# Kernel tuning notes

Hardware: AMD Instinct MI355X
Metric: run time of the kernel (lower is better)

## Reference

```python
import jax, jax.numpy as jnp
import numpy as np

B, T, D, H, O = 256, 512, 256, 1024, 128


def setup_inputs() -> dict:
    key = jax.random.key(0)
    ks = jax.random.split(key, 16)
    s_x = 1.0 / np.sqrt(D)
    s_h = 1.0 / np.sqrt(H)
    def lin(k, shape, s):
        return jax.random.uniform(k, shape, jnp.float32, -s, s)
    return {
        "x": jax.random.normal(ks[0], (B, T, D), jnp.float32),
        "Wgx": lin(ks[1], (H, D), s_x), "bgx": lin(ks[2], (H,), s_x),
        "Wgh": lin(ks[3], (H, H), s_h),
        "Wix": lin(ks[4], (H, D), s_x), "bix": lin(ks[5], (H,), s_x),
        "Wih": lin(ks[6], (H, H), s_h),
        "Wfx": lin(ks[7], (H, D), s_x), "bfx": lin(ks[8], (H,), s_x),
        "Wfh": lin(ks[9], (H, H), s_h),
        "Wox": lin(ks[10], (H, D), s_x), "box": lin(ks[11], (H,), s_x),
        "Woh": lin(ks[12], (H, H), s_h),
        "Why": lin(ks[13], (O, H), s_h), "bhy": lin(ks[14], (O,), s_h),
    }


def _lstm_forward(x, Wgx, bgx, Wgh, Wix, bix, Wih, Wfx, bfx, Wfh, Wox, box, Woh, Why, bhy):
    # Precompute all input-side projections in one big GEMM: [B,T,4H]
    Wx = jnp.concatenate([Wgx, Wix, Wfx, Wox], axis=0)          # [4H, D]
    bx = jnp.concatenate([bgx, bix, bfx, box], axis=0)          # [4H]
    Wh = jnp.concatenate([Wgh, Wih, Wfh, Woh], axis=0)          # [4H, H]
    xz = jnp.einsum('btd,kd->tbk', x, Wx) + bx                  # [T,B,4H]

    Hd = Wgh.shape[0]

    def step(carry, xz_t):
        h, c = carry
        z = xz_t + h @ Wh.T                                     # [B,4H]
        g = jnp.tanh(z[:, :Hd])
        i = jax.nn.sigmoid(z[:, Hd:2 * Hd])
        f = jax.nn.sigmoid(z[:, 2 * Hd:3 * Hd])
        o = jax.nn.sigmoid(z[:, 3 * Hd:])
        c = g * i + c * f
        h = jnp.tanh(c) * o
        return (h, c), None

    h0 = jnp.zeros((x.shape[0], Hd), x.dtype)
    c0 = jnp.zeros((x.shape[0], Hd), x.dtype)
    (h, _), _ = jax.lax.scan(step, (h0, c0), xz)
    p = h @ Why.T + bhy
    return jax.nn.softmax(p, axis=-1)


def reference(x, Wgx, bgx, Wgh, Wix, bix, Wih, Wfx, bfx, Wfh, Wox, box, Woh, Why, bhy):
    return _lstm_forward(x, Wgx, bgx, Wgh, Wix, bix, Wih, Wfx, bfx, Wfh, Wox, box, Woh, Why, bhy)
```

## Files before the change

### kernel.cpp

```cpp
#include <hip/hip_runtime.h>
#include <math.h>

#define B_  256
#define T_  512
#define D_  256
#define H_  1024
#define O_  128
#define N4H 4096

typedef __attribute__((ext_vector_type(8))) short bf16x8;
typedef __attribute__((ext_vector_type(4))) float f32x4;

__device__ __forceinline__ unsigned short f2bf(float x) {
    union { float f; unsigned u; } v; v.f = x;
    unsigned r = v.u + 0x7fffu + ((v.u >> 16) & 1u);
    return (unsigned short)(r >> 16);
}
__device__ __forceinline__ float bf2f(unsigned short b) {
    union { float f; unsigned u; } v; v.u = ((unsigned)b) << 16;
    return v.f;
}
__device__ __forceinline__ void splitf(float w, short& hi, short& lo) {
    union { float f; unsigned u; } v; v.f = w;
    union { float f; unsigned u; } hf; hf.u = v.u & 0xffff0000u;
    hi = (short)(unsigned short)(v.u >> 16);
    lo = (short)f2bf(w - hf.f);
}

__global__ __launch_bounds__(256) void pack_weights(
    const float* __restrict__ Wgx, const float* __restrict__ bgx, const float* __restrict__ Wgh,
    const float* __restrict__ Wix, const float* __restrict__ bix, const float* __restrict__ Wih,
    const float* __restrict__ Wfx, const float* __restrict__ bfx, const float* __restrict__ Wfh,
    const float* __restrict__ Wox, const float* __restrict__ box, const float* __restrict__ Woh,
    unsigned short* __restrict__ Whhi, unsigned short* __restrict__ Whlo,
    unsigned short* __restrict__ WXhi, unsigned short* __restrict__ WXlo,
    float* __restrict__ biasP)
{
    int idx = blockIdx.x * 256 + threadIdx.x;
    const int K = H_ + D_;
    const int total = N4H * K;
    if (idx < total) {
        int np = idx / K;
        int k  = idx - np * K;
        int j = np >> 2, g = np & 3;
        const float* Wh = (g == 0) ? Wgh : (g == 1) ? Wih : (g == 2) ? Wfh : Woh;
        const float* Wx = (g == 0) ? Wgx : (g == 1) ? Wix : (g == 2) ? Wfx : Wox;
        float w = (k < H_) ? Wh[j * H_ + k] : Wx[j * D_ + (k - H_)];
        unsigned short hi = f2bf(w);
        unsigned short lo = f2bf(w - bf2f(hi));
        if (k < H_) { Whhi[np * H_ + k] = hi; Whlo[np * H_ + k] = lo; }
        else        { WXhi[np * D_ + (k - H_)] = hi; WXlo[np * D_ + (k - H_)] = lo; }
    }
    if (idx < N4H) {
        int j = idx >> 2, g = idx & 3;
        const float* bx = (g == 0) ? bgx : (g == 1) ? bix : (g == 2) ? bfx : box;
        biasP[idx] = bx[j];
    }
}

__global__ __launch_bounds__(256, 2) void xz_gemm(
    const float* __restrict__ x,
    const unsigned short* __restrict__ WXhi, const unsigned short* __restrict__ WXlo,
    const float* __restrict__ biasP,
    float* __restrict__ xz, int t0)
{
    const int tid  = threadIdx.x;
    const int wave = tid >> 6;
    const int lane = tid & 63;
    const int lrow = lane & 15;
    const int quad = lane >> 4;
    const int wr = wave >> 1, wc = wave & 1;

    const int cg    = blockIdx.x;
    const int t_rel = blockIdx.y >> 1;
    const int bhalf = blockIdx.y & 1;
    const int t     = t0 + t_rel;

    const int b0 = bhalf * 128 + wr * 64;
    const int n0 = cg * 128 + wc * 64;

    f32x4 acc[4][4];
    #pragma unroll
    for (int rs = 0; rs < 4; ++rs)
        #pragma unroll
        for (int cs = 0; cs < 4; ++cs)
            acc[rs][cs] = (f32x4){0.f, 0.f, 0.f, 0.f};

    #pragma unroll 1
    for (int kc = 0; kc < D_; kc += 32) {
        bf16x8 Ahi[4], Alo[4], Bh[4], Bl[4];
        #pragma unroll
        for (int rs = 0; rs < 4; ++rs) {
            int b = b0 + rs * 16 + lrow;
            const float* p = x + (size_t)b * (T_ * D_) + (size_t)t * D_ + kc + quad * 8;
            float4 v0 = *(const float4*)p;
            float4 v1 = *(const float4*)(p + 4);
            float vv[8] = {v0.x, v0.y, v0.z, v0.w, v1.x, v1.y, v1.z, v1.w};
            #pragma unroll
            for (int j = 0; j < 8; ++j) {
                short hi, lo; splitf(vv[j], hi, lo);
                Ahi[rs][j] = hi; Alo[rs][j] = lo;
            }
        }
        #pragma unroll
        for (int cs = 0; cs < 4; ++cs) {
            int rw = n0 + cs * 16 + lrow;
            int off = rw * D_ + kc + quad * 8;
            Bh[cs] = *(const bf16x8*)(WXhi + off);
            Bl[cs] = *(const bf16x8*)(WXlo + off);
        }
        #pragma unroll
        for (int rs = 0; rs < 4; ++rs)
            #pragma unroll
            for (int cs = 0; cs < 4; ++cs) {
                acc[rs][cs] = __builtin_amdgcn_mfma_f32_16x16x32_bf16(Ahi[rs], Bh[cs], acc[rs][cs], 0, 0, 0);
                acc[rs][cs] = __builtin_amdgcn_mfma_f32_16x16x32_bf16(Ahi[rs], Bl[cs], acc[rs][cs], 0, 0, 0);
                acc[rs][cs] = __builtin_amdgcn_mfma_f32_16x16x32_bf16(Alo[rs], Bh[cs], acc[rs][cs], 0, 0, 0);
            }
    }

    #pragma unroll
    for (int cs = 0; cs < 4; ++cs) {
        int col = n0 + cs * 16 + lrow;
        float bv = biasP[col];
        #pragma unroll
        for (int rs = 0; rs < 4; ++rs) {
            int row0 = b0 + rs * 16 + quad * 4;
            #pragma unroll
            for (int r = 0; r < 4; ++r)
                xz[(size_t)(t_rel * B_ + row0 + r) * N4H + col] = acc[rs][cs][r] + bv;
        }
    }
}

__global__ __launch_bounds__(512, 2) void lstm_step(
    const unsigned short* __restrict__ Whhi, const unsigned short* __restrict__ Whlo,
    const unsigned short* __restrict__ hin_hi, const unsigned short* __restrict__ hin_lo,
    unsigned short* __restrict__ hout_hi, unsigned short* __restrict__ hout_lo,
    float* __restrict__ cst, const float* __restrict__ xz, int t_rel)
{
    __shared__ __align__(16) float zbuf[8][64][68];

    const int tid  = threadIdx.x;
    const int wave = tid >> 6;
    const int lane = tid & 63;
    const int lrow = lane & 15;
    const int quad = lane >> 4;

    const int fid = blockIdx.x;
    const int xcd = fid & 7;
    const int s   = fid >> 3;
    const int cg  = xcd * 8 + (s & 7);
    const int rg  = s >> 3;
    const int rbase = rg * 64;
    const int cbase = cg * 64;

    f32x4 acc[4][4];
    #pragma unroll
    for (int rs = 0; rs < 4; ++rs)
        #pragma unroll
        for (int cs = 0; cs < 4; ++cs)
            acc[rs][cs] = (f32x4){0.f, 0.f, 0.f, 0.f};

    const int kb = wave * 128;
    #pragma unroll 2
    for (int kc = 0; kc < 128; kc += 32) {
        const int k = kb + kc + quad * 8;
        bf16x8 Ahi[4], Alo[4], Bh[4], Bl[4];
        #pragma unroll
        for (int rs = 0; rs < 4; ++rs) {
            int off = (rbase + rs * 16 + lrow) * H_ + k;
            Ahi[rs] = *(const bf16x8*)(hin_hi + off);
            Alo[rs] = *(const bf16x8*)(hin_lo + off);
        }
        #pragma unroll
        for (int cs = 0; cs < 4; ++cs) {
            int off = (cbase + cs * 16 + lrow) * H_ + k;
            Bh[cs] = *(const bf16x8*)(Whhi + off);
            Bl[cs] = *(const bf16x8*)(Whlo + off);
        }
        #pragma unroll
        for (int rs = 0; rs < 4; ++rs)
            #pragma unroll
            for (int cs = 0; cs < 4; ++cs) {
                acc[rs][cs] = __builtin_amdgcn_mfma_f32_16x16x32_bf16(Ahi[rs], Bh[cs], acc[rs][cs], 0, 0, 0);
                acc[rs][cs] = __builtin_amdgcn_mfma_f32_16x16x32_bf16(Ahi[rs], Bl[cs], acc[rs][cs], 0, 0, 0);
                acc[rs][cs] = __builtin_amdgcn_mfma_f32_16x16x32_bf16(Alo[rs], Bh[cs], acc[rs][cs], 0, 0, 0);
            }
    }

    #pragma unroll
    for (int rs = 0; rs < 4; ++rs)
        #pragma unroll
        for (int cs = 0; cs < 4; ++cs)
            #pragma unroll
            for (int r = 0; r < 4; ++r)
                zbuf[wave][rs * 16 + quad * 4 + r][cs * 16 + lrow] = acc[rs][cs][r];
    __syncthreads();

    const int b_loc = tid >> 3;
    const int oc    = (tid & 7) * 8;

    float zz[8];
    #pragma unroll
    for (int i = 0; i < 8; i += 4) {
        float s0 = 0.f, s1 = 0.f, s2 = 0.f, s3 = 0.f;
        #pragma unroll
        for (int w = 0; w < 8; ++w) {
            float4 v = *(const float4*)&zbuf[w][b_loc][oc + i];
            s0 += v.x; s1 += v.y; s2 += v.z; s3 += v.w;
        }
        zz[i] = s0; zz[i + 1] = s1; zz[i + 2] = s2; zz[i + 3] = s3;
    }

    const int b = rbase + b_loc;
    const size_t xzoff = ((size_t)t_rel * B_ + b) * N4H + cbase + oc;
    float4 xa = *(const float4*)(xz + xzoff);
    float4 xb = *(const float4*)(xz + xzoff + 4);
    zz[0] += xa.x; zz[1] += xa.y; zz[2] += xa.z; zz[3] += xa.w;
    zz[4] += xb.x; zz[5] += xb.y; zz[6] += xb.z; zz[7] += xb.w;

    const int j0 = cg * 16 + (tid & 7) * 2;
    float2 cold = *(const float2*)&cst[b * H_ + j0];
    float coldv[2] = {cold.x, cold.y};

    float cnew[2];
    unsigned short hh[2], hl[2];
    #pragma unroll
    for (int j = 0; j < 2; ++j) {
        float zg = zz[4 * j + 0];
        float zi = zz[4 * j + 1];
        float zf = zz[4 * j + 2];
        float zo = zz[4 * j + 3];
        float g  = tanhf(zg);
        float ig = 1.f / (1.f + expf(-zi));
        float fg = 1.f / (1.f + expf(-zf));
        float og = 1.f / (1.f + expf(-zo));
        float cn = g * ig + coldv[j] * fg;
        float hn = tanhf(cn) * og;
        cnew[j] = cn;
        unsigned short h16 = f2bf(hn);
        hh[j] = h16;
        hl[j] = f2bf(hn - bf2f(h16));
    }
    *(float2*)&cst[b * H_ + j0] = make_float2(cnew[0], cnew[1]);
    *(ushort2*)&hout_hi[b * H_ + j0] = make_ushort2(hh[0], hh[1]);
    *(ushort2*)&hout_lo[b * H_ + j0] = make_ushort2(hl[0], hl[1]);
}

__global__ __launch_bounds__(128) void final_proj(
    const unsigned short* __restrict__ hhi, const unsigned short* __restrict__ hlo,
    const float* __restrict__ Why, const float* __restrict__ bhy,
    float* __restrict__ out)
{
    __shared__ float hsh[H_];
    __shared__ float red[O_];
    const int b = blockIdx.x, tid = threadIdx.x;

    for (int k = tid; k < H_; k += O_)
        hsh[k] = bf2f(hhi[(size_t)b * H_ + k]) + bf2f(hlo[(size_t)b * H_ + k]);
    __syncthreads();

    float s = bhy[tid];
    const float* w = Why + (size_t)tid * H_;
    #pragma unroll 4
    for (int k = 0; k < H_; k += 4) {
        float4 wv = *(const float4*)(w + k);
        s += hsh[k] * wv.x + hsh[k + 1] * wv.y + hsh[k + 2] * wv.z + hsh[k + 3] * wv.w;
    }

    red[tid] = s; __syncthreads();
    for (int off = 64; off > 0; off >>= 1) {
        if (tid < off) red[tid] = fmaxf(red[tid], red[tid + off]);
        __syncthreads();
    }
    float mx = red[0]; __syncthreads();
    float e = expf(s - mx);
    red[tid] = e; __syncthreads();
    for (int off = 64; off > 0; off >>= 1) {
        if (tid < off) red[tid] += red[tid + off];
        __syncthreads();
    }
    out[(size_t)b * O_ + tid] = e / red[0];
}

extern "C" void kernel_launch(void* const* d_in, const int* in_sizes, int n_in,
                              void* d_out, int out_size, void* d_ws, size_t ws_size,
                              hipStream_t stream)
{
    const float* x   = (const float*)d_in[0];
    const float* Wgx = (const float*)d_in[1];
    const float* bgx = (const float*)d_in[2];
    const float* Wgh = (const float*)d_in[3];
    const float* Wix = (const float*)d_in[4];
    const float* bix = (const float*)d_in[5];
    const float* Wih = (const float*)d_in[6];
    const float* Wfx = (const float*)d_in[7];
    const float* bfx = (const float*)d_in[8];
    const float* Wfh = (const float*)d_in[9];
    const float* Wox = (const float*)d_in[10];
    const float* box = (const float*)d_in[11];
    const float* Woh = (const float*)d_in[12];
    const float* Why = (const float*)d_in[13];
    const float* bhy = (const float*)d_in[14];

    unsigned short* Whhi = (unsigned short*)d_ws;
    unsigned short* Whlo = Whhi + (size_t)N4H * H_;
    unsigned short* WXhi = Whlo + (size_t)N4H * H_;
    unsigned short* WXlo = WXhi + (size_t)N4H * D_;
    float*          bP   = (float*)(WXlo + (size_t)N4H * D_);
    unsigned short* hA_hi = (unsigned short*)(bP + N4H);
    unsigned short* hA_lo = hA_hi + (size_t)B_ * H_;
    float*          cst   = (float*)(hA_lo + (size_t)B_ * H_);
    unsigned short* hB_hi = (unsigned short*)(cst + (size_t)B_ * H_);
    unsigned short* hB_lo = hB_hi + (size_t)B_ * H_;
    float*          xz    = (float*)(hB_lo + (size_t)B_ * H_);

    const size_t fixed_bytes = (size_t)((char*)xz - (char*)d_ws);
    const size_t per_t = (size_t)B_ * N4H * sizeof(float);
    int Tc = 1;
    if (ws_size > fixed_bytes) {
        size_t fit = (ws_size - fixed_bytes) / per_t;
        Tc = (fit > 64) ? 64 : (fit < 1 ? 1 : (int)fit);
    }

    hipMemsetAsync(hA_hi, 0, (size_t)B_ * H_ * 8, stream);

    const int totalW = N4H * (H_ + D_);
    pack_weights<<<(totalW + 255) / 256, 256, 0, stream>>>(
        Wgx, bgx, Wgh, Wix, bix, Wih, Wfx, bfx, Wfh, Wox, box, Woh,
        Whhi, Whlo, WXhi, WXlo, bP);

    for (int t0 = 0; t0 < T_; t0 += Tc) {
        const int tc = (T_ - t0 < Tc) ? (T_ - t0) : Tc;
        xz_gemm<<<dim3(32, 2 * tc), 256, 0, stream>>>(x, WXhi, WXlo, bP, xz, t0);
        for (int t = t0; t < t0 + tc; ++t) {
            const unsigned short* ih = (t & 1) ? hB_hi : hA_hi;
            const unsigned short* il = (t & 1) ? hB_lo : hA_lo;
            unsigned short* oh = (t & 1) ? hA_hi : hB_hi;
            unsigned short* ol = (t & 1) ? hA_lo : hB_lo;
            lstm_step<<<256, 512, 0, stream>>>(
                Whhi, Whlo, ih, il, oh, ol, cst, xz, t - t0);
        }
    }

    final_proj<<<B_, 128, 0, stream>>>(hA_hi, hA_lo, Why, bhy, (float*)d_out);
}
```

Baseline: 11.96 ms.

## Fuse LSTM timesteps and input GEMM into persistent cooperative kernel

Replaces the per-chunk input-projection launches and the per-timestep step launches with one cooperative persistent kernel. Each block first computes the input projections for its own batch-row and gate-column tile, then loops over timesteps. Steps are separated by a global-memory atomic barrier that only spans the 64 blocks sharing a batch-row group, since the recurrence never mixes batch rows. The cell state now stays in registers instead of round-tripping through global memory. The aim is to remove kernel launch and inter-kernel drain overhead. In exchange it adds spin-wait barrier latency, and it relies on all 256 blocks being co-resident.

```diff
diff --git a/kernel.cpp b/kernel.cpp
--- a/kernel.cpp
+++ b/kernel.cpp
@@ -58,194 +58,205 @@
     }
 }
 
-__global__ __launch_bounds__(256, 2) void xz_gemm(
+__global__ __launch_bounds__(512, 2) void lstm_persistent(
     const float* __restrict__ x,
+    const unsigned short* __restrict__ Whhi, const unsigned short* __restrict__ Whlo,
     const unsigned short* __restrict__ WXhi, const unsigned short* __restrict__ WXlo,
     const float* __restrict__ biasP,
-    float* __restrict__ xz, int t0)
+    unsigned short* __restrict__ h0hi, unsigned short* __restrict__ h0lo,
+    unsigned short* __restrict__ h1hi, unsigned short* __restrict__ h1lo,
+    float* __restrict__ xz,
+    unsigned int* __restrict__ bar,
+    int Tc)
 {
+    __shared__ __align__(16) float zbuf[8][64][68];
+
     const int tid  = threadIdx.x;
     const int wave = tid >> 6;
     const int lane = tid & 63;
     const int lrow = lane & 15;
     const int quad = lane >> 4;
-    const int wr = wave >> 1, wc = wave & 1;
-
-    const int cg    = blockIdx.x;
-    const int t_rel = blockIdx.y >> 1;
-    const int bhalf = blockIdx.y & 1;
-    const int t     = t0 + t_rel;
-
-    const int b0 = bhalf * 128 + wr * 64;
-    const int n0 = cg * 128 + wc * 64;
-
-    f32x4 acc[4][4];
-    #pragma unroll
-    for (int rs = 0; rs < 4; ++rs)
-        #pragma unroll
-        for (int cs = 0; cs < 4; ++cs)
-            acc[rs][cs] = (f32x4){0.f, 0.f, 0.f, 0.f};
-
-    #pragma unroll 1
-    for (int kc = 0; kc < D_; kc += 32) {
-        bf16x8 Ahi[4], Alo[4], Bh[4], Bl[4];
-        #pragma unroll
-        for (int rs = 0; rs < 4; ++rs) {
-            int b = b0 + rs * 16 + lrow;
-            const float* p = x + (size_t)b * (T_ * D_) + (size_t)t * D_ + kc + quad * 8;
-            float4 v0 = *(const float4*)p;
-            float4 v1 = *(const float4*)(p + 4);
-            float vv[8] = {v0.x, v0.y, v0.z, v0.w, v1.x, v1.y, v1.z, v1.w};
-            #pragma unroll
-            for (int j = 0; j < 8; ++j) {
-                short hi, lo; splitf(vv[j], hi, lo);
-                Ahi[rs][j] = hi; Alo[rs][j] = lo;
-            }
-        }
-        #pragma unroll
-        for (int cs = 0; cs < 4; ++cs) {
-            int rw = n0 + cs * 16 + lrow;
-            int off = rw * D_ + kc + quad * 8;
-            Bh[cs] = *(const bf16x8*)(WXhi + off);
-            Bl[cs] = *(const bf16x8*)(WXlo + off);
-        }
-        #pragma unroll
-        for (int rs = 0; rs < 4; ++rs)
-            #pragma unroll
-            for (int cs = 0; cs < 4; ++cs) {
-                acc[rs][cs] = __builtin_amdgcn_mfma_f32_16x16x32_bf16(Ahi[rs], Bh[cs], acc[rs][cs], 0, 0, 0);
-                acc[rs][cs] = __builtin_amdgcn_mfma_f32_16x16x32_bf16(Ahi[rs], Bl[cs], acc[rs][cs], 0, 0, 0);
-                acc[rs][cs] = __builtin_amdgcn_mfma_f32_16x16x32_bf16(Alo[rs], Bh[cs], acc[rs][cs], 0, 0, 0);
-            }
-    }
-
-    #pragma unroll
-    for (int cs = 0; cs < 4; ++cs) {
-        int col = n0 + cs * 16 + lrow;
-        float bv = biasP[col];
-        #pragma unroll
-        for (int rs = 0; rs < 4; ++rs) {
-            int row0 = b0 + rs * 16 + quad * 4;
-            #pragma unroll
-            for (int r = 0; r < 4; ++r)
-                xz[(size_t)(t_rel * B_ + row0 + r) * N4H + col] = acc[rs][cs][r] + bv;
-        }
-    }
-}
-
-__global__ __launch_bounds__(512, 2) void lstm_step(
-    const unsigned short* __restrict__ Whhi, const unsigned short* __restrict__ Whlo,
-    const unsigned short* __restrict__ hin_hi, const unsigned short* __restrict__ hin_lo,
-    unsigned short* __restrict__ hout_hi, unsigned short* __restrict__ hout_lo,
-    float* __restrict__ cst, const float* __restrict__ xz, int t_rel)
-{
-    __shared__ __align__(16) float zbuf[8][64][68];
-
-    const int tid  = threadIdx.x;
-    const int wave = tid >> 6;
-    const int lane = tid & 63;
-    const int lrow = lane & 15;
-    const int quad = lane >> 4;
 
     const int fid = blockIdx.x;
     const int xcd = fid & 7;
     const int s   = fid >> 3;
-    const int cg  = xcd * 8 + (s & 7);
+    const int cgi = xcd * 8 + (s & 7);
     const int rg  = s >> 3;
     const int rbase = rg * 64;
-    const int cbase = cg * 64;
-
-    f32x4 acc[4][4];
-    #pragma unroll
-    for (int rs = 0; rs < 4; ++rs)
-        #pragma unroll
-        for (int cs = 0; cs < 4; ++cs)
-            acc[rs][cs] = (f32x4){0.f, 0.f, 0.f, 0.f};
-
-    const int kb = wave * 128;
-    #pragma unroll 2
-    for (int kc = 0; kc < 128; kc += 32) {
-        const int k = kb + kc + quad * 8;
-        bf16x8 Ahi[4], Alo[4], Bh[4], Bl[4];
-        #pragma unroll
-        for (int rs = 0; rs < 4; ++rs) {
-            int off = (rbase + rs * 16 + lrow) * H_ + k;
-            Ahi[rs] = *(const bf16x8*)(hin_hi + off);
-            Alo[rs] = *(const bf16x8*)(hin_lo + off);
-        }
-        #pragma unroll
-        for (int cs = 0; cs < 4; ++cs) {
-            int off = (cbase + cs * 16 + lrow) * H_ + k;
-            Bh[cs] = *(const bf16x8*)(Whhi + off);
-            Bl[cs] = *(const bf16x8*)(Whlo + off);
-        }
-        #pragma unroll
-        for (int rs = 0; rs < 4; ++rs)
-            #pragma unroll
-            for (int cs = 0; cs < 4; ++cs) {
-                acc[rs][cs] = __builtin_amdgcn_mfma_f32_16x16x32_bf16(Ahi[rs], Bh[cs], acc[rs][cs], 0, 0, 0);
-                acc[rs][cs] = __builtin_amdgcn_mfma_f32_16x16x32_bf16(Ahi[rs], Bl[cs], acc[rs][cs], 0, 0, 0);
-                acc[rs][cs] = __builtin_amdgcn_mfma_f32_16x16x32_bf16(Alo[rs], Bh[cs], acc[rs][cs], 0, 0, 0);
-            }
-    }
-
-    #pragma unroll
-    for (int rs = 0; rs < 4; ++rs)
-        #pragma unroll
-        for (int cs = 0; cs < 4; ++cs)
-            #pragma unroll
-            for (int r = 0; r < 4; ++r)
-                zbuf[wave][rs * 16 + quad * 4 + r][cs * 16 + lrow] = acc[rs][cs][r];
-    __syncthreads();
+    const int cbase = cgi * 64;
 
     const int b_loc = tid >> 3;
     const int oc    = (tid & 7) * 8;
-
-    float zz[8];
-    #pragma unroll
-    for (int i = 0; i < 8; i += 4) {
-        float s0 = 0.f, s1 = 0.f, s2 = 0.f, s3 = 0.f;
-        #pragma unroll
-        for (int w = 0; w < 8; ++w) {
-            float4 v = *(const float4*)&zbuf[w][b_loc][oc + i];
-            s0 += v.x; s1 += v.y; s2 += v.z; s3 += v.w;
+    const int bown  = rbase + b_loc;
+    const int j0    = cgi * 16 + (tid & 7) * 2;
+    float c0 = 0.f, c1 = 0.f;
+
+    unsigned int* const mybar = bar + rg * 32;
+    unsigned int barTarget = 0;
+
+    for (int t0 = 0; t0 < T_; t0 += Tc) {
+        const int tc = (T_ - t0 < Tc) ? (T_ - t0) : Tc;
+
+        for (int t_rel = wave; t_rel < tc; t_rel += 8) {
+            const int t = t0 + t_rel;
+            f32x4 acc[4][4];
+            #pragma unroll
+            for (int rs = 0; rs < 4; ++rs)
+                #pragma unroll
+                for (int cs = 0; cs < 4; ++cs)
+                    acc[rs][cs] = (f32x4){0.f, 0.f, 0.f, 0.f};
+
+            #pragma unroll 1
+            for (int kc = 0; kc < D_; kc += 32) {
+                bf16x8 Ahi[4], Alo[4], Bh[4], Bl[4];
+                #pragma unroll
+                for (int rs = 0; rs < 4; ++rs) {
+                    int b = rbase + rs * 16 + lrow;
+                    const float* p = x + (size_t)b * (T_ * D_) + (size_t)t * D_ + kc + quad * 8;
+                    float4 v0 = *(const float4*)p;
+                    float4 v1 = *(const float4*)(p + 4);
+                    float vv[8] = {v0.x, v0.y, v0.z, v0.w, v1.x, v1.y, v1.z, v1.w};
+                    #pragma unroll
+                    for (int j = 0; j < 8; ++j) {
+                        short hi, lo; splitf(vv[j], hi, lo);
+                        Ahi[rs][j] = hi; Alo[rs][j] = lo;
+                    }
+                }
+                #pragma unroll
+                for (int cs = 0; cs < 4; ++cs) {
+                    int off = (cbase + cs * 16 + lrow) * D_ + kc + quad * 8;
+                    Bh[cs] = *(const bf16x8*)(WXhi + off);
+                    Bl[cs] = *(const bf16x8*)(WXlo + off);
+                }
+                #pragma unroll
+                for (int rs = 0; rs < 4; ++rs)
+                    #pragma unroll
+                    for (int cs = 0; cs < 4; ++cs) {
+                        acc[rs][cs] = __builtin_amdgcn_mfma_f32_16x16x32_bf16(Ahi[rs], Bh[cs], acc[rs][cs], 0, 0, 0);
+                        acc[rs][cs] = __builtin_amdgcn_mfma_f32_16x16x32_bf16(Ahi[rs], Bl[cs], acc[rs][cs], 0, 0, 0);
+                        acc[rs][cs] = __builtin_amdgcn_mfma_f32_16x16x32_bf16(Alo[rs], Bh[cs], acc[rs][cs], 0, 0, 0);
+                    }
+            }
+            #pragma unroll
+            for (int cs = 0; cs < 4; ++cs) {
+                int col = cbase + cs * 16 + lrow;
+                float bv = biasP[col];
+                #pragma unroll
+                for (int rs = 0; rs < 4; ++rs) {
+                    int row0 = rbase + rs * 16 + quad * 4;
+                    #pragma unroll
+                    for (int r = 0; r < 4; ++r)
+                        xz[(size_t)(t_rel * B_ + row0 + r) * N4H + col] = acc[rs][cs][r] + bv;
+                }
+            }
         }
-        zz[i] = s0; zz[i + 1] = s1; zz[i + 2] = s2; zz[i + 3] = s3;
-    }
-
-    const int b = rbase + b_loc;
-    const size_t xzoff = ((size_t)t_rel * B_ + b) * N4H + cbase + oc;
-    float4 xa = *(const float4*)(xz + xzoff);
-    float4 xb = *(const float4*)(xz + xzoff + 4);
-    zz[0] += xa.x; zz[1] += xa.y; zz[2] += xa.z; zz[3] += xa.w;
-    zz[4] += xb.x; zz[5] += xb.y; zz[6] += xb.z; zz[7] += xb.w;
-
-    const int j0 = cg * 16 + (tid & 7) * 2;
-    float2 cold = *(const float2*)&cst[b * H_ + j0];
-    float coldv[2] = {cold.x, cold.y};
-
-    float cnew[2];
-    unsigned short hh[2], hl[2];
-    #pragma unroll
-    for (int j = 0; j < 2; ++j) {
-        float zg = zz[4 * j + 0];
-        float zi = zz[4 * j + 1];
-        float zf = zz[4 * j + 2];
-        float zo = zz[4 * j + 3];
-        float g  = tanhf(zg);
-        float ig = 1.f / (1.f + expf(-zi));
-        float fg = 1.f / (1.f + expf(-zf));
-        float og = 1.f / (1.f + expf(-zo));
-        float cn = g * ig + coldv[j] * fg;
-        float hn = tanhf(cn) * og;
-        cnew[j] = cn;
-        unsigned short h16 = f2bf(hn);
-        hh[j] = h16;
-        hl[j] = f2bf(hn - bf2f(h16));
-    }
-    *(float2*)&cst[b * H_ + j0] = make_float2(cnew[0], cnew[1]);
-    *(ushort2*)&hout_hi[b * H_ + j0] = make_ushort2(hh[0], hh[1]);
-    *(ushort2*)&hout_lo[b * H_ + j0] = make_ushort2(hl[0], hl[1]);
+
+        for (int t_rel = 0; t_rel < tc; ++t_rel) {
+            const int t = t0 + t_rel;
+            const unsigned short* ih = (t & 1) ? h1hi : h0hi;
+            const unsigned short* il = (t & 1) ? h1lo : h0lo;
+            unsigned short* oh = (t & 1) ? h0hi : h1hi;
+            unsigned short* ol = (t & 1) ? h0lo : h1lo;
+
+            f32x4 acc[4][4];
+            #pragma unroll
+            for (int rs = 0; rs < 4; ++rs)
+                #pragma unroll
+                for (int cs = 0; cs < 4; ++cs)
+                    acc[rs][cs] = (f32x4){0.f, 0.f, 0.f, 0.f};
+
+            const int kb = wave * 128;
+            #pragma unroll 2
+            for (int kc = 0; kc < 128; kc += 32) {
+                const int k = kb + kc + quad * 8;
+                bf16x8 Ahi[4], Alo[4], Bh[4], Bl[4];
+                #pragma unroll
+                for (int rs = 0; rs < 4; ++rs) {
+                    int off = (rbase + rs * 16 + lrow) * H_ + k;
+                    Ahi[rs] = *(const bf16x8*)(ih + off);
+                    Alo[rs] = *(const bf16x8*)(il + off);
+                }
+                #pragma unroll
+                for (int cs = 0; cs < 4; ++cs) {
+                    int off = (cbase + cs * 16 + lrow) * H_ + k;
+                    Bh[cs] = *(const bf16x8*)(Whhi + off);
+                    Bl[cs] = *(const bf16x8*)(Whlo + off);
+                }
+                #pragma unroll
+                for (int rs = 0; rs < 4; ++rs)
+                    #pragma unroll
+                    for (int cs = 0; cs < 4; ++cs) {
+                        acc[rs][cs] = __builtin_amdgcn_mfma_f32_16x16x32_bf16(Ahi[rs], Bh[cs], acc[rs][cs], 0, 0, 0);
+                        acc[rs][cs] = __builtin_amdgcn_mfma_f32_16x16x32_bf16(Ahi[rs], Bl[cs], acc[rs][cs], 0, 0, 0);
+                        acc[rs][cs] = __builtin_amdgcn_mfma_f32_16x16x32_bf16(Alo[rs], Bh[cs], acc[rs][cs], 0, 0, 0);
+                    }
+            }
+
+            #pragma unroll
+            for (int rs = 0; rs < 4; ++rs)
+                #pragma unroll
+                for (int cs = 0; cs < 4; ++cs)
+                    #pragma unroll
+                    for (int r = 0; r < 4; ++r)
+                        zbuf[wave][rs * 16 + quad * 4 + r][cs * 16 + lrow] = acc[rs][cs][r];
+            __syncthreads();
+
+            float zz[8];
+            #pragma unroll
+            for (int i = 0; i < 8; i += 4) {
+                float s0 = 0.f, s1 = 0.f, s2 = 0.f, s3 = 0.f;
+                #pragma unroll
+                for (int w = 0; w < 8; ++w) {
+                    float4 v = *(const float4*)&zbuf[w][b_loc][oc + i];
+                    s0 += v.x; s1 += v.y; s2 += v.z; s3 += v.w;
+                }
+                zz[i] = s0; zz[i + 1] = s1; zz[i + 2] = s2; zz[i + 3] = s3;
+            }
+
+            const size_t xzoff = ((size_t)t_rel * B_ + bown) * N4H + cbase + oc;
+            float4 xa = *(const float4*)(xz + xzoff);
+            float4 xb = *(const float4*)(xz + xzoff + 4);
+            zz[0] += xa.x; zz[1] += xa.y; zz[2] += xa.z; zz[3] += xa.w;
+            zz[4] += xb.x; zz[5] += xb.y; zz[6] += xb.z; zz[7] += xb.w;
+
+            float cold[2] = {c0, c1};
+            unsigned short hh[2], hl[2];
+            float cnew[2];
+            #pragma unroll
+            for (int j = 0; j < 2; ++j) {
+                float zg = zz[4 * j + 0];
+                float zi = zz[4 * j + 1];
+                float zf = zz[4 * j + 2];
+                float zo = zz[4 * j + 3];
+                float g  = tanhf(zg);
+                float ig = 1.f / (1.f + expf(-zi));
+                float fg = 1.f / (1.f + expf(-zf));
+                float og = 1.f / (1.f + expf(-zo));
+                float cn = g * ig + cold[j] * fg;
+                float hn = tanhf(cn) * og;
+                cnew[j] = cn;
+                unsigned short h16 = f2bf(hn);
+                hh[j] = h16;
+                hl[j] = f2bf(hn - bf2f(h16));
+            }
+            c0 = cnew[0]; c1 = cnew[1];
+            *(ushort2*)&oh[bown * H_ + j0] = make_ushort2(hh[0], hh[1]);
+            *(ushort2*)&ol[bown * H_ + j0] = make_ushort2(hl[0], hl[1]);
+
+            if (t != T_ - 1) {
+                barTarget += 64;
+                if (tid == 0) {
+                    __threadfence();
+                    atomicAdd(mybar, 1u);
+                    while (__hip_atomic_load(mybar, __ATOMIC_RELAXED,
+                                             __HIP_MEMORY_SCOPE_AGENT) < barTarget)
+                        __builtin_amdgcn_s_sleep(1);
+                    __threadfence();
+                }
+            }
+            __syncthreads();
+        }
+    }
 }
 
 __global__ __launch_bounds__(128) void final_proj(
@@ -309,10 +320,10 @@
     unsigned short* WXhi = Whlo + (size_t)N4H * H_;
     unsigned short* WXlo = WXhi + (size_t)N4H * D_;
     float*          bP   = (float*)(WXlo + (size_t)N4H * D_);
-    unsigned short* hA_hi = (unsigned short*)(bP + N4H);
+    unsigned int*   bars = (unsigned int*)(bP + N4H);
+    unsigned short* hA_hi = (unsigned short*)(bars + 128);
     unsigned short* hA_lo = hA_hi + (size_t)B_ * H_;
-    float*          cst   = (float*)(hA_lo + (size_t)B_ * H_);
-    unsigned short* hB_hi = (unsigned short*)(cst + (size_t)B_ * H_);
+    unsigned short* hB_hi = hA_lo + (size_t)B_ * H_;
     unsigned short* hB_lo = hB_hi + (size_t)B_ * H_;
     float*          xz    = (float*)(hB_lo + (size_t)B_ * H_);
 
@@ -324,25 +335,20 @@
         Tc = (fit > 64) ? 64 : (fit < 1 ? 1 : (int)fit);
     }
 
-    hipMemsetAsync(hA_hi, 0, (size_t)B_ * H_ * 8, stream);
+    hipMemsetAsync(bars, 0, 512 + (size_t)B_ * H_ * 4, stream);
 
     const int totalW = N4H * (H_ + D_);
     pack_weights<<<(totalW + 255) / 256, 256, 0, stream>>>(
         Wgx, bgx, Wgh, Wix, bix, Wih, Wfx, bfx, Wfh, Wox, box, Woh,
         Whhi, Whlo, WXhi, WXlo, bP);
 
-    for (int t0 = 0; t0 < T_; t0 += Tc) {
-        const int tc = (T_ - t0 < Tc) ? (T_ - t0) : Tc;
-        xz_gemm<<<dim3(32, 2 * tc), 256, 0, stream>>>(x, WXhi, WXlo, bP, xz, t0);
-        for (int t = t0; t < t0 + tc; ++t) {
-            const unsigned short* ih = (t & 1) ? hB_hi : hA_hi;
-            const unsigned short* il = (t & 1) ? hB_lo : hA_lo;
-            unsigned short* oh = (t & 1) ? hA_hi : hB_hi;
-            unsigned short* ol = (t & 1) ? hA_lo : hB_lo;
-            lstm_step<<<256, 512, 0, stream>>>(
-                Whhi, Whlo, ih, il, oh, ol, cst, xz, t - t0);
-        }
-    }
+    void* kargs[] = {
+        (void*)&x, (void*)&Whhi, (void*)&Whlo, (void*)&WXhi, (void*)&WXlo,
+        (void*)&bP, (void*)&hA_hi, (void*)&hA_lo, (void*)&hB_hi, (void*)&hB_lo,
+        (void*)&xz, (void*)&bars, (void*)&Tc
+    };
+    hipLaunchCooperativeKernel((const void*)lstm_persistent,
+                               dim3(256), dim3(512), kargs, 0, stream);
 
     final_proj<<<B_, 128, 0, stream>>>(hA_hi, hA_lo, Why, bhy, (float*)d_out);
 }
```

After: 18.99 ms. 58.8% more time.
